# Kernel optimization log

Measured on AMD Instinct MI355X. Metric: run time of the kernel, lower is better.

The kernel has to match this reference:

```python
import math
import jax, jax.numpy as jnp
import numpy as np
from jax.scipy.special import gammaln, xlogy

B, N1, N2 = 4, 2048, 512
D, H, DK = 768, 8, 64
DV = D // H        # 96 (dim_value = dim // heads)
NRP = D // H       # 96 num_rel_pos_features (divisible by 6)
DY0 = 1280 + 256   # esm_dim + cell_line_dim
EPS = 1e-5
SCALE = DK ** -0.5


def layer_norm(z, g, b):
    m = jnp.mean(z, -1, keepdims=True)
    v = jnp.mean(jnp.square(z - m), -1, keepdims=True)
    return (z - m) * jax.lax.rsqrt(v + EPS) * g + b


def get_positional_embed(seq_len, feature_size):
    # Enformer-style relative positional features over distances [-(L-1), L-1]
    d = jnp.arange(-seq_len + 1, seq_len)
    ad = jnp.abs(d).astype(jnp.float32)[:, None]  # [2L-1, 1]
    nb = feature_size // 6
    # exponential half-life basis
    max_range = math.log(seq_len) / math.log(2.0)
    half_life = 2.0 ** jnp.linspace(3.0, max_range, nb)
    f_exp = jnp.exp(-math.log(2.0) / half_life * ad)
    # central mask basis
    cw = 2.0 ** jnp.arange(1, nb + 1).astype(jnp.float32) - 1.0
    f_cm = (cw > ad).astype(jnp.float32)
    # gamma pdf basis
    stddev = seq_len / (2.0 * nb)
    start_mean = seq_len / nb
    mean = jnp.linspace(start_mean, float(seq_len), nb)
    conc = (mean / stddev) ** 2
    rate = mean / (stddev ** 2)
    logp = xlogy(conc - 1.0, ad) - rate * ad - (gammaln(conc) - conc * jnp.log(rate))
    prob = jnp.exp(logp) + 1e-8
    f_g = prob / jnp.max(prob, -1, keepdims=True)
    emb = jnp.concatenate([f_exp, f_cm, f_g], -1)  # [2L-1, feature_size/2]
    sign = jnp.sign(d).astype(jnp.float32)[:, None]
    return jnp.concatenate([emb, sign * emb], -1)  # [2L-1, feature_size]


def relative_shift(z):
    # Transformer-XL shift: [b,h,i,2*L-1] -> [b,h,i,L]
    b, h, i, j = z.shape
    z = jnp.pad(z, ((0, 0), (0, 0), (0, 0), (1, 0)))
    z = z.reshape(b, h, j + 1, i)[:, :, 1:, :].reshape(b, h, i, j)
    return z[..., : (j + 2) // 2]


def ffn(z, g, b, w1, b1, w2, b2):
    h = layer_norm(z, g, b)
    h = jax.nn.relu(h @ w1 + b1)
    return z + h @ w2 + b2


def setup_inputs() -> dict:
    key = jax.random.key(0)
    ks = jax.random.split(key, 32)
    p = lambda i, shape, s=0.02: jax.random.normal(ks[i], shape, jnp.float32) * s
    return dict(
        x=jax.random.normal(ks[0], (B, N1, D), jnp.float32),
        y0=jax.random.normal(ks[1], (B, N2, DY0), jnp.float32),
        W_res=p(2, (DY0, D)),
        lnx_g=jnp.ones((D,)), lnx_b=jnp.zeros((D,)),
        lny_g=jnp.ones((D,)), lny_b=jnp.zeros((D,)),
        Wq=p(3, (D, H * DK)), Wk=p(4, (D, H * DK)),
        Wv1=p(5, (D, H * DV)), Wv2=p(6, (D, H * DV)),
        Wo1=p(7, (H * DV, D)), bo1=jnp.zeros((D,)),
        Wo2=p(8, (H * DV, D)), bo2=jnp.zeros((D,)),
        Wrel=p(9, (NRP, H * DK)),
        rel_pos_bias=p(10, (H, DK), 1.0),
        fx_g=jnp.ones((D,)), fx_b=jnp.zeros((D,)),
        fx_w1=p(11, (D, 2 * D)), fx_b1=jnp.zeros((2 * D,)),
        fx_w2=p(12, (2 * D, D)), fx_b2=jnp.zeros((D,)),
        fy_g=jnp.ones((D,)), fy_b=jnp.zeros((D,)),
        fy_w1=p(13, (D, 2 * D)), fy_b1=jnp.zeros((2 * D,)),
        fy_w2=p(14, (2 * D, D)), fy_b2=jnp.zeros((D,)),
    )


def reference(x, y0, W_res, lnx_g, lnx_b, lny_g, lny_b, Wq, Wk, Wv1, Wv2,
              Wo1, bo1, Wo2, bo2, Wrel, rel_pos_bias,
              fx_g, fx_b, fx_w1, fx_b1, fx_w2, fx_b2,
              fy_g, fy_b, fy_w1, fy_b1, fy_w2, fy_b2):
    b, n1, _ = x.shape
    n2 = y0.shape[1]
    y = y0 @ W_res                               # res_proj (first layer)
    x1 = layer_norm(x, lnx_g, lnx_b)
    y1 = layer_norm(y, lny_g, lny_b)

    q = (x1 @ Wq).reshape(b, n1, H, DK).transpose(0, 2, 1, 3) * SCALE
    k = (y1 @ Wk).reshape(b, n2, H, DK).transpose(0, 2, 1, 3)
    v2 = (y1 @ Wv2).reshape(b, n2, H, DV).transpose(0, 2, 1, 3)

    content = jnp.einsum('bhid,bhjd->bhij', q, k)  # [b,h,n1,n2]

    pos = get_positional_embed(n1, NRP)            # [2*n1-1, NRP]
    rel_q = (pos @ Wrel).reshape(2 * n1 - 1, H, DK).transpose(1, 0, 2)
    kb = k * SCALE + rel_pos_bias[None, :, None, :]
    rel = jnp.einsum('bhjd,hmd->bhjm', kb, rel_q)  # [b,h,n2,2*n1-1]
    rel = relative_shift(rel)                      # [b,h,n2,n1]
    logits = content + rel.transpose(0, 1, 3, 2)

    attn = jax.nn.softmax(logits, -1)
    out1 = jnp.einsum('bhij,bhjd->bhid', attn, v2)
    out1 = out1.transpose(0, 2, 1, 3).reshape(b, n1, H * DV)
    x2 = out1 @ Wo1 + bo1

    v1 = (x1 @ Wv1).reshape(b, n1, H, DV).transpose(0, 2, 1, 3)
    out2 = jnp.einsum('bhij,bhid->bhjd', attn, v1)  # attn^T @ v1
    out2 = out2.transpose(0, 2, 1, 3).reshape(b, n2, H * DV)
    y2 = out2 @ Wo2 + bo2

    x4 = x + x2
    x5 = ffn(x4, fx_g, fx_b, fx_w1, fx_b1, fx_w2, fx_b2)
    y4 = y2 + y
    y5 = ffn(y4, fy_g, fy_b, fy_w1, fy_b1, fy_w2, fy_b2)
    return (x5, y5)
```

## Files before the change

kernel.cpp:

```cpp
#include <hip/hip_runtime.h>
#include <hip/hip_bf16.h>
#include <math.h>

typedef __hip_bfloat16 bf16;
typedef short s16x8 __attribute__((ext_vector_type(8)));
typedef short s16x4 __attribute__((ext_vector_type(4)));
typedef float f32x4 __attribute__((ext_vector_type(4)));

#define B_    4
#define N1_   2048
#define N2_   512
#define D_    768
#define H_    8
#define DK_   64
#define DV_   96
#define NPOS_ 4095
#define SCALE_ 0.125f

__device__ __forceinline__ float b2f(bf16 v) { return __bfloat162float(v); }
__device__ __forceinline__ bf16  f2b(float v) { return __float2bfloat16(v); }
__device__ __forceinline__ float us2f(unsigned short u) {
    return __uint_as_float(((unsigned int)u) << 16);
}
__device__ __forceinline__ unsigned short f2bu(float v) {
    bf16 t = __float2bfloat16(v);
    return *reinterpret_cast<unsigned short*>(&t);
}
__device__ __forceinline__ float ldf(const float* p) { return *p; }
__device__ __forceinline__ float ldf(const bf16* p)  { return __bfloat162float(*p); }
__device__ __forceinline__ void stf(float* p, float v) { *p = v; }
__device__ __forceinline__ void stf(bf16* p, float v)  { *p = f2b(v); }
#define MFMA16(a, b, c) __builtin_amdgcn_mfma_f32_16x16x32_bf16((a), (b), (c), 0, 0, 0)

__device__ __forceinline__ void gl16(const unsigned short* g, unsigned short* l) {
    __builtin_amdgcn_global_load_lds(
        (const __attribute__((address_space(1))) unsigned int*)g,
        (__attribute__((address_space(3))) unsigned int*)l, 16, 0, 0);
}

struct PackT {
    const float* src[12];
    unsigned K[12], N[12], dbase[12], drow[12];
    unsigned t0[13];
};

__global__ __launch_bounds__(256) void packT_kernel(PackT pa, bf16* __restrict__ dst)
{
    int bid = blockIdx.x, s = 0;
    while (s < 11 && bid >= (int)pa.t0[s + 1]) s++;
    int t = bid - (int)pa.t0[s];
    unsigned K = pa.K[s], N = pa.N[s];
    unsigned ntk = K >> 5;
    unsigned k0 = (t % ntk) << 5, n0 = (t / ntk) << 6;
    __shared__ float tile[32][65];
    const float* src = pa.src[s];
    int tid = threadIdx.x;
    {
        int e = tid * 8, k = e >> 6, n = e & 63;
        const float* p = src + (size_t)(k0 + k) * N + n0 + n;
#pragma unroll
        for (int j = 0; j < 8; j++) tile[k][n + j] = p[j];
    }
    __syncthreads();
    {
        int f = tid * 8, n = f >> 5, k = f & 31;
        bf16* q = dst + (size_t)pa.dbase[s] + (size_t)(n0 + n) * pa.drow[s] + k0 + k;
#pragma unroll
        for (int j = 0; j < 8; j++) q[j] = f2b(tile[k + j][n]);
    }
}

__global__ __launch_bounds__(256) void cvt8_kernel(
    const float* __restrict__ in, bf16* __restrict__ out)
{
    int i = (blockIdx.x * 256 + threadIdx.x) * 8;
    f32x4 a = *reinterpret_cast<const f32x4*>(in + i);
    f32x4 b = *reinterpret_cast<const f32x4*>(in + i + 4);
    s16x8 w;
#pragma unroll
    for (int j = 0; j < 4; j++) {
        w[j] = (short)f2bu(a[j]);
        w[4 + j] = (short)f2bu(b[j]);
    }
    *reinterpret_cast<s16x8*>((unsigned short*)out + i) = w;
}

template <typename T>
__global__ __launch_bounds__(64) void lnfull_kernel(
    const T* __restrict__ in, const float* __restrict__ g,
    const float* __restrict__ b, bf16* __restrict__ out)
{
    int row = blockIdx.x, lane = threadIdx.x;
    const T* p = in + (size_t)row * D_;
    float v[12];
    float s = 0.f;
#pragma unroll
    for (int i = 0; i < 12; i++) { v[i] = ldf(p + lane + i * 64); s += v[i]; }
#pragma unroll
    for (int o = 32; o > 0; o >>= 1) s += __shfl_down(s, o);
    float mean = __shfl(s, 0) * (1.f / 768.f);
    float var = 0.f;
#pragma unroll
    for (int i = 0; i < 12; i++) { float d = v[i] - mean; var += d * d; }
#pragma unroll
    for (int o = 32; o > 0; o >>= 1) var += __shfl_down(var, o);
    float rstd = rsqrtf(__shfl(var, 0) * (1.f / 768.f) + 1e-5f);
    bf16* q = out + (size_t)row * D_;
#pragma unroll
    for (int i = 0; i < 12; i++) {
        int c = lane + i * 64;
        q[c] = f2b((v[i] - mean) * rstd * g[c] + b[c]);
    }
}

__global__ __launch_bounds__(256, 4) void wres_splitk_kernel(
    const bf16* __restrict__ Av, const bf16* __restrict__ BwT,
    float* __restrict__ Cp)
{
    __shared__ __align__(16) unsigned short As[128 * 64];
    __shared__ __align__(16) unsigned short Bs[128 * 64];
    const int K = 1536;
    int tid = threadIdx.x, wave = tid >> 6, lane = tid & 63;
    int lc = lane & 15, kq = lane >> 4;
    int wm = (wave & 1) * 64, wn = (wave >> 1) * 64;
    int bid = blockIdx.x;
    int sbid = (bid & 7) * 48 + (bid >> 3);
    int s = sbid / 96, t = sbid % 96;
    int bm = (t / 6) * 128, bn = (t % 6) * 128;
    int ks = s * 384;
    f32x4 acc[4][4] = {};
    int grow = tid >> 3, gcol = (tid & 7) * 8;
    const unsigned short* ag = (const unsigned short*)Av + (size_t)(bm + grow) * K + gcol;
    const unsigned short* bg = (const unsigned short*)BwT + (size_t)(bn + grow) * K + gcol;
    unsigned short* asl = As + wave * 512;
    unsigned short* bsl = Bs + wave * 512;

    for (int k0 = ks; k0 < ks + 384; k0 += 64) {
#pragma unroll
        for (int it = 0; it < 4; it++) {
            gl16(ag + (size_t)(it * 32) * K + k0, asl + it * 2048);
            gl16(bg + (size_t)(it * 32) * K + k0, bsl + it * 2048);
        }
        __syncthreads();
#pragma unroll
        for (int kh = 0; kh < 2; kh++) {
            s16x8 af[4], bf[4];
#pragma unroll
            for (int mt = 0; mt < 4; mt++)
                af[mt] = *reinterpret_cast<const s16x8*>(&As[(wm + mt * 16 + lc) * 64 + kh * 32 + kq * 8]);
#pragma unroll
            for (int nt = 0; nt < 4; nt++)
                bf[nt] = *reinterpret_cast<const s16x8*>(&Bs[(wn + nt * 16 + lc) * 64 + kh * 32 + kq * 8]);
#pragma unroll
            for (int mt = 0; mt < 4; mt++)
#pragma unroll
                for (int nt = 0; nt < 4; nt++)
                    acc[mt][nt] = MFMA16(af[mt], bf[nt], acc[mt][nt]);
        }
        __syncthreads();
    }

    float* out = Cp + (size_t)s * (2048 * 768);
#pragma unroll
    for (int mt = 0; mt < 4; mt++)
#pragma unroll
        for (int nt = 0; nt < 4; nt++) {
            int n = bn + wn + nt * 16 + lc;
#pragma unroll
            for (int r = 0; r < 4; r++) {
                int m = bm + wm + mt * 16 + kq * 4 + r;
                out[(size_t)m * 768 + n] = acc[mt][nt][r];
            }
        }
}

__global__ __launch_bounds__(64) void lnred4_kernel(
    const float* __restrict__ Cp, const float* __restrict__ g,
    const float* __restrict__ b, float* __restrict__ yb, bf16* __restrict__ y1)
{
    int row = blockIdx.x, lane = threadIdx.x;
    const size_t SL = (size_t)2048 * 768;
    const float* p = Cp + (size_t)row * 768;
    float* yo = yb + (size_t)row * 768;
    float v[12];
    float s = 0.f;
#pragma unroll
    for (int i = 0; i < 12; i++) {
        int c = lane + i * 64;
        float t = p[c] + p[SL + c] + p[2 * SL + c] + p[3 * SL + c];
        v[i] = t; s += t;
        yo[c] = t;
    }
#pragma unroll
    for (int o = 32; o > 0; o >>= 1) s += __shfl_down(s, o);
    float mean = __shfl(s, 0) * (1.f / 768.f);
    float var = 0.f;
#pragma unroll
    for (int i = 0; i < 12; i++) { float d = v[i] - mean; var += d * d; }
#pragma unroll
    for (int o = 32; o > 0; o >>= 1) var += __shfl_down(var, o);
    float rstd = rsqrtf(__shfl(var, 0) * (1.f / 768.f) + 1e-5f);
    bf16* q = y1 + (size_t)row * D_;
#pragma unroll
    for (int i = 0; i < 12; i++) {
        int c = lane + i * 64;
        q[c] = f2b((v[i] - mean) * rstd * g[c] + b[c]);
    }
}

template <int AM, typename TC, typename TR>
__device__ __forceinline__ void gemm128_body(
    unsigned short* As, unsigned short* Bs, int tid,
    const void* Av, const bf16* BwT, TC* C, int M, int N, int K,
    const float* bias, int relu, const TR* res,
    bf16* Cq, bf16* Cv, bf16* Cq2, const float* qbias2,
    float sscale, int vshift, int bm, int bn)
{
    int wave = tid >> 6, lane = tid & 63;
    int lc = lane & 15, kq = lane >> 4;
    int wm = (wave & 1) * 64, wn = (wave >> 1) * 64;
    f32x4 acc[4][4] = {};
    int grow = tid >> 3, gcol = (tid & 7) * 8;
    const unsigned short* bg = (const unsigned short*)BwT + (size_t)(bn + grow) * K + gcol;
    unsigned short* asl = As + wave * 512;
    unsigned short* bsl = Bs + wave * 512;
    const size_t SL = (size_t)B_ * N2_ * 768;

    for (int k0 = 0; k0 < K; k0 += 64) {
        if (AM == 0) {
            const unsigned short* ag = (const unsigned short*)Av + (size_t)(bm + grow) * K + k0 + gcol;
#pragma unroll
            for (int it = 0; it < 4; it++)
                gl16(ag + (size_t)(it * 32) * K, asl + it * 2048);
        } else {
#pragma unroll
            for (int it = 0; it < 4; it++) {
                const unsigned short* a0 = (const unsigned short*)Av
                    + (size_t)(bm + grow + it * 32) * K + k0 + gcol;
                s16x8 v0 = *reinterpret_cast<const s16x8*>(a0);
                s16x8 v1 = *reinterpret_cast<const s16x8*>(a0 + SL);
                s16x8 v2 = *reinterpret_cast<const s16x8*>(a0 + 2 * SL);
                s16x8 v3 = *reinterpret_cast<const s16x8*>(a0 + 3 * SL);
                s16x8 w;
#pragma unroll
                for (int j = 0; j < 8; j++)
                    w[j] = (short)f2bu(us2f((unsigned short)v0[j]) + us2f((unsigned short)v1[j]) +
                                       us2f((unsigned short)v2[j]) + us2f((unsigned short)v3[j]));
                *reinterpret_cast<s16x8*>(&As[(grow + it * 32) * 64 + gcol]) = w;
            }
        }
#pragma unroll
        for (int it = 0; it < 4; it++)
            gl16(bg + (size_t)(it * 32) * K + k0, bsl + it * 2048);
        __syncthreads();
#pragma unroll
        for (int kh = 0; kh < 2; kh++) {
            s16x8 af[4], bf[4];
#pragma unroll
            for (int mt = 0; mt < 4; mt++)
                af[mt] = *reinterpret_cast<const s16x8*>(&As[(wm + mt * 16 + lc) * 64 + kh * 32 + kq * 8]);
#pragma unroll
            for (int nt = 0; nt < 4; nt++)
                bf[nt] = *reinterpret_cast<const s16x8*>(&Bs[(wn + nt * 16 + lc) * 64 + kh * 32 + kq * 8]);
#pragma unroll
            for (int mt = 0; mt < 4; mt++)
#pragma unroll
                for (int nt = 0; nt < 4; nt++)
                    acc[mt][nt] = MFMA16(af[mt], bf[nt], acc[mt][nt]);
        }
        __syncthreads();
    }

#pragma unroll
    for (int mt = 0; mt < 4; mt++) {
#pragma unroll
        for (int nt = 0; nt < 4; nt++) {
            int n = bn + wn + nt * 16 + lc;
            float bv = (!Cq && bias) ? bias[n] : 0.f;
#pragma unroll
            for (int r = 0; r < 4; r++) {
                int m = bm + wm + mt * 16 + kq * 4 + r;
                float vr = acc[mt][nt][r];
                if (Cq) {
                    int rows = 1 << vshift;
                    int bb = m >> vshift, rr = m & (rows - 1);
                    if (n < 512) {
                        size_t off = (((size_t)bb * 8 + (n >> 6)) * rows + rr) * 64 + (n & 63);
                        Cq[off] = f2b(vr * sscale);
                        if (Cq2) Cq2[off] = f2b(vr * SCALE_ + qbias2[n]);
                    } else {
                        int nn = n - 512, hh = nn / 96, dv = nn - hh * 96;
                        Cv[(((size_t)bb * 8 + hh) * rows + rr) * 96 + dv] = f2b(vr);
                    }
                } else {
                    float v = vr + bv;
                    if (relu) v = fmaxf(v, 0.f);
                    size_t off = (size_t)m * N + n;
                    if (res) v += ldf(res + off);
                    stf(C + off, v);
                }
            }
        }
    }
}

struct GP {
    const void* Av; const bf16* BwT; void* C;
    int M, N, K;
    const float* bias; int relu; const void* res;
    bf16 *Cq, *Cv, *Cq2; const float* qbias2;
    float sscale; int vshift; int nbx, nwg;
};

template <int AMA, int AMB, typename TC, typename TR>
__global__ __launch_bounds__(256, 4) void dual128_kernel(GP a, GP b)
{
    __shared__ __align__(16) unsigned short As[128 * 64];
    __shared__ __align__(16) unsigned short Bs[128 * 64];
    int tid = threadIdx.x;
    int bid = blockIdx.x;
    if (bid < a.nwg) {
        int sbid = (a.nwg & 7) ? bid : ((bid & 7) * (a.nwg >> 3) + (bid >> 3));
        gemm128_body<AMA, TC, TR>(As, Bs, tid, a.Av, a.BwT, (TC*)a.C,
            a.M, a.N, a.K, a.bias, a.relu, (const TR*)a.res,
            a.Cq, a.Cv, a.Cq2, a.qbias2, a.sscale, a.vshift,
            (sbid / a.nbx) * 128, (sbid % a.nbx) * 128);
    } else {
        int lb = bid - a.nwg;
        int sbid = (b.nwg & 7) ? lb : ((lb & 7) * (b.nwg >> 3) + (lb >> 3));
        gemm128_body<AMB, TC, TR>(As, Bs, tid, b.Av, b.BwT, (TC*)b.C,
            b.M, b.N, b.K, b.bias, b.relu, (const TR*)b.res,
            b.Cq, b.Cv, b.Cq2, b.qbias2, b.sscale, b.vshift,
            (sbid / b.nbx) * 128, (sbid % b.nbx) * 128);
    }
}

__global__ __launch_bounds__(256, 4) void dual3_kernel(GP a, GP b,
    const bf16* __restrict__ relA, const bf16* __restrict__ relB,
    bf16* __restrict__ relC)
{
    __shared__ __align__(16) unsigned short As[128 * 64];
    __shared__ __align__(16) unsigned short Bs[128 * 64];
    int tid = threadIdx.x;
    int bid = blockIdx.x;
    if (bid < a.nwg) {
        int sbid = (bid & 7) * (a.nwg >> 3) + (bid >> 3);
        gemm128_body<0, bf16, float>(As, Bs, tid, a.Av, a.BwT, (bf16*)a.C,
            a.M, a.N, a.K, a.bias, a.relu, (const float*)a.res,
            a.Cq, a.Cv, a.Cq2, a.qbias2, a.sscale, a.vshift,
            (sbid / a.nbx) * 128, (sbid % a.nbx) * 128);
    } else if (bid < a.nwg + b.nwg) {
        int lb = bid - a.nwg;
        int sbid = (lb & 7) * (b.nwg >> 3) + (lb >> 3);
        gemm128_body<0, bf16, float>(As, Bs, tid, b.Av, b.BwT, (bf16*)b.C,
            b.M, b.N, b.K, b.bias, b.relu, (const float*)b.res,
            b.Cq, b.Cv, b.Cq2, b.qbias2, b.sscale, b.vshift,
            (sbid / b.nbx) * 128, (sbid % b.nbx) * 128);
    } else {
        int lb = bid - a.nwg - b.nwg;
        int slb = (lb & 7) * 64 + (lb >> 3);
        int bm = (slb >> 3) * 64, bn = (slb & 7) * 64;
        const int M = NPOS_, N = 512, K = 96;
        unsigned short (*A6)[40] = (unsigned short (*)[40])As;
        unsigned short (*B6)[40] = (unsigned short (*)[40])Bs;
        int wave = tid >> 6, lane = tid & 63;
        f32x4 acc[4] = {};
        int am = tid >> 2, ak = (tid & 3) * 8;
        int bn_ = tid & 63, bk = (tid >> 6) * 8;
        for (int k0 = 0; k0 < K; k0 += 32) {
            s16x8 va = {};
            if (bm + am < M)
                va = *reinterpret_cast<const s16x8*>(
                    (const unsigned short*)relA + (size_t)(bm + am) * K + k0 + ak);
            *reinterpret_cast<s16x8*>(&A6[am][ak]) = va;
            *reinterpret_cast<s16x8*>(&B6[bn_][bk]) =
                *reinterpret_cast<const s16x8*>(
                    (const unsigned short*)relB + (size_t)(bn + bn_) * K + k0 + bk);
            __syncthreads();
            s16x8 af = *reinterpret_cast<const s16x8*>(&A6[wave * 16 + (lane & 15)][(lane >> 4) * 8]);
#pragma unroll
            for (int ns = 0; ns < 4; ns++) {
                s16x8 bf = *reinterpret_cast<const s16x8*>(&B6[ns * 16 + (lane & 15)][(lane >> 4) * 8]);
                acc[ns] = MFMA16(af, bf, acc[ns]);
            }
            __syncthreads();
        }
        int col = lane & 15, rg = (lane >> 4) * 4;
#pragma unroll
        for (int ns = 0; ns < 4; ns++) {
            int n = bn + ns * 16 + col;
#pragma unroll
            for (int r = 0; r < 4; r++) {
                int m = bm + wave * 16 + rg + r;
                if (m < M) relC[(size_t)m * N + n] = f2b(acc[ns][r]);
            }
        }
    }
}

__global__ __launch_bounds__(64) void pos_kernel(bf16* __restrict__ pos)
{
    int m = blockIdx.x * 64 + threadIdx.x;
    if (m >= NPOS_) return;
    float dist = (float)(m - 2047);
    float ad = fabsf(dist);
    float sgn = (dist > 0.f) ? 1.f : ((dist < 0.f) ? -1.f : 0.f);
    float f[48];
#pragma unroll
    for (int t = 0; t < 16; t++) {
        float hl = exp2f(3.f + (8.f / 15.f) * (float)t);
        f[t] = expf(-0.69314718056f / hl * ad);
    }
#pragma unroll
    for (int t = 0; t < 16; t++) {
        float cw = exp2f((float)(t + 1)) - 1.f;
        f[16 + t] = (cw > ad) ? 1.f : 0.f;
    }
    float pr[16];
    float mx = 0.f;
    if (ad < 0.5f) {
#pragma unroll
        for (int t = 0; t < 16; t++) pr[t] = 1e-8f;
        mx = 1e-8f;
    } else {
        float lad = logf(ad);
#pragma unroll
        for (int t = 0; t < 16; t++) {
            float mean = 128.f * (float)(t + 1);
            float cc = (mean / 64.f) * (mean / 64.f);
            float rate = mean * (1.f / 4096.f);
            float logp = (cc - 1.f) * lad - rate * ad - (lgammaf(cc) - cc * logf(rate));
            float p = expf(logp) + 1e-8f;
            pr[t] = p;
            mx = fmaxf(mx, p);
        }
    }
#pragma unroll
    for (int t = 0; t < 16; t++) f[32 + t] = pr[t] / mx;

    bf16* o = pos + (size_t)m * 96;
#pragma unroll
    for (int c = 0; c < 48; c++) { o[c] = f2b(f[c]); o[48 + c] = f2b(sgn * f[c]); }
}

#define TP_ 344
__global__ __launch_bounds__(256) void tshift_kernel(
    const bf16* __restrict__ kbb, const bf16* __restrict__ relq,
    bf16* __restrict__ tsh, int base, int plen)
{
    int mc = blockIdx.x, jt = blockIdx.y, bh = blockIdx.z;
    int mbase = mc << 8, jg0 = jt << 6, h = bh & 7;
    int iwin0 = mbase + jg0 - 511 - base;
    if (iwin0 + 318 < 0 || iwin0 >= plen) return;
    int a0 = iwin0 & 7;
    int iwa = iwin0 - a0;
    __shared__ unsigned short Tl[64][TP_];
    int tid = threadIdx.x, wave = tid >> 6, lane = tid & 63;
    int lc = lane & 15, kq = lane >> 4;

    const bf16* ap = kbb + ((size_t)bh * N2_ + jg0 + wave * 16 + lc) * 64 + kq * 8;
    s16x8 af0 = *reinterpret_cast<const s16x8*>(ap);
    s16x8 af1 = *reinterpret_cast<const s16x8*>(ap + 32);

    int jrow = wave * 16 + kq * 4;
#pragma unroll
    for (int sub = 0; sub < 2; sub++) {
        int m0 = mbase + sub * 128;
        f32x4 tacc[8] = {};
#pragma unroll
        for (int ns = 0; ns < 8; ns++) {
            const bf16* rp = relq + (size_t)(m0 + ns * 16 + lc) * 512 + h * 64 + kq * 8;
            s16x8 rf0 = *reinterpret_cast<const s16x8*>(rp);
            s16x8 rf1 = *reinterpret_cast<const s16x8*>(rp + 32);
            tacc[ns] = MFMA16(af0, rf0, tacc[ns]);
            tacc[ns] = MFMA16(af1, rf1, tacc[ns]);
        }
#pragma unroll
        for (int ns = 0; ns < 8; ns++)
#pragma unroll
            for (int r = 0; r < 4; r++) {
                int col = sub * 128 + ns * 16 + lc + jrow + r + a0;
                Tl[jrow + r][col] = f2bu(tacc[ns][r]);
            }
    }
    __syncthreads();

    int row = tid >> 2, q = tid & 3;
    int cstart = row + a0;
    bf16* out = tsh + ((size_t)bh * N2_ + jg0 + row) * (size_t)plen;
#pragma unroll
    for (int s = 0; s < 11; s++) {
        int c = (q + s * 4) * 8;
        int i = iwa + c;
        if (c >= cstart && c + 8 <= cstart + 256 && i >= 0 && i + 8 <= plen) {
            *reinterpret_cast<s16x8*>(out + i) =
                *reinterpret_cast<const s16x8*>(&Tl[row][c]);
        } else {
#pragma unroll
            for (int e = 0; e < 8; e++) {
                int ce = c + e, ie = i + e;
                if (ce >= cstart && ce < cstart + 256 && ie >= 0 && ie < plen)
                    out[ie] = *reinterpret_cast<const bf16*>(&Tl[row][ce]);
            }
        }
    }
}

__global__ __launch_bounds__(256) void attn1_kernel(
    const bf16* __restrict__ qb, const bf16* __restrict__ kb,
    const bf16* __restrict__ tsh, const bf16* __restrict__ v2,
    bf16* __restrict__ out1, float* __restrict__ mst, float* __restrict__ lst,
    int base, int tpitch)
{
    int bh = blockIdx.y;
    int b = bh >> 3, h = bh & 7;
    int i0 = base + blockIdx.x * 64;
    __shared__ __align__(16) unsigned short Ts[64][72];
    __shared__ __align__(16) unsigned short Ps[64][72];
    __shared__ __align__(16) unsigned short Vs[96][72];
    int tid = threadIdx.x, wave = tid >> 6, lane = tid & 63;
    int lc = lane & 15, kq = lane >> 4;
    int ibase = wave * 16 + kq * 4;

    const bf16* qp = qb + ((size_t)bh * N1_ + i0 + wave * 16 + lc) * 64 + kq * 8;
    s16x8 qf0 = *reinterpret_cast<const s16x8*>(qp);
    s16x8 qf1 = *reinterpret_cast<const s16x8*>(qp + 32);

    int trow = tid >> 2, tchunk = tid & 3;
    const unsigned short* tb0 = (const unsigned short*)tsh
        + ((size_t)bh * N2_ + trow) * tpitch + (i0 - base) + tchunk * 16;
    const unsigned short* vb0 = (const unsigned short*)v2
        + ((size_t)bh * N2_ + trow) * 96 + tchunk * 24;

    float m_run[4], l_run[4];
#pragma unroll
    for (int r = 0; r < 4; r++) { m_run[r] = -1e30f; l_run[r] = 0.f; }
    f32x4 oacc[6] = {};

    for (int j0 = 0; j0 < N2_; j0 += 64) {
        __syncthreads();
        {
            const unsigned short* p = tb0 + (size_t)j0 * tpitch;
            *reinterpret_cast<s16x8*>(&Ts[trow][tchunk * 16]) =
                *reinterpret_cast<const s16x8*>(p);
            *reinterpret_cast<s16x8*>(&Ts[trow][tchunk * 16 + 8]) =
                *reinterpret_cast<const s16x8*>(p + 8);
        }
        {
            const unsigned short* p = vb0 + (size_t)j0 * 96;
            s16x8 w0 = *reinterpret_cast<const s16x8*>(p);
            s16x8 w1 = *reinterpret_cast<const s16x8*>(p + 8);
            s16x8 w2 = *reinterpret_cast<const s16x8*>(p + 16);
            int vd = tchunk * 24;
#pragma unroll
            for (int s = 0; s < 8; s++) Vs[vd + s][trow] = (unsigned short)w0[s];
#pragma unroll
            for (int s = 0; s < 8; s++) Vs[vd + 8 + s][trow] = (unsigned short)w1[s];
#pragma unroll
            for (int s = 0; s < 8; s++) Vs[vd + 16 + s][trow] = (unsigned short)w2[s];
        }
        __syncthreads();

        f32x4 cacc[4] = {};
#pragma unroll
        for (int ns = 0; ns < 4; ns++) {
            const bf16* kp = kb + ((size_t)bh * N2_ + j0 + ns * 16 + lc) * 64 + kq * 8;
            s16x8 kf0 = *reinterpret_cast<const s16x8*>(kp);
            s16x8 kf1 = *reinterpret_cast<const s16x8*>(kp + 32);
            cacc[ns] = MFMA16(qf0, kf0, cacc[ns]);
            cacc[ns] = MFMA16(qf1, kf1, cacc[ns]);
        }
        float Lv[4][4];
#pragma unroll
        for (int ns = 0; ns < 4; ns++) {
            int jloc = ns * 16 + lc;
            s16x4 tv = *reinterpret_cast<const s16x4*>(&Ts[jloc][ibase]);
#pragma unroll
            for (int r = 0; r < 4; r++)
                Lv[ns][r] = cacc[ns][r] + us2f((unsigned short)tv[r]);
        }
#pragma unroll
        for (int r = 0; r < 4; r++) {
            float v = fmaxf(fmaxf(Lv[0][r], Lv[1][r]), fmaxf(Lv[2][r], Lv[3][r]));
            v = fmaxf(v, __shfl_xor(v, 1));
            v = fmaxf(v, __shfl_xor(v, 2));
            v = fmaxf(v, __shfl_xor(v, 4));
            v = fmaxf(v, __shfl_xor(v, 8));
            float mn = fmaxf(m_run[r], v);
            float alpha = __expf(m_run[r] - mn);
            m_run[r] = mn;
            float s = 0.f;
#pragma unroll
            for (int ns = 0; ns < 4; ns++) {
                float p = __expf(Lv[ns][r] - mn);
                Lv[ns][r] = p;
                s += p;
            }
            s += __shfl_xor(s, 1);
            s += __shfl_xor(s, 2);
            s += __shfl_xor(s, 4);
            s += __shfl_xor(s, 8);
            l_run[r] = l_run[r] * alpha + s;
#pragma unroll
            for (int ns6 = 0; ns6 < 6; ns6++) oacc[ns6][r] *= alpha;
        }
#pragma unroll
        for (int ns = 0; ns < 4; ns++)
#pragma unroll
            for (int r = 0; r < 4; r++)
                Ps[ibase + r][ns * 16 + lc] = f2bu(Lv[ns][r]);
#pragma unroll
        for (int kk = 0; kk < 2; kk++) {
            s16x8 pf = *reinterpret_cast<const s16x8*>(&Ps[wave * 16 + lc][kq * 8 + kk * 32]);
#pragma unroll
            for (int ns6 = 0; ns6 < 6; ns6++) {
                s16x8 vf = *reinterpret_cast<const s16x8*>(&Vs[ns6 * 16 + lc][kq * 8 + kk * 32]);
                oacc[ns6] = MFMA16(pf, vf, oacc[ns6]);
            }
        }
    }

    float invl[4];
#pragma unroll
    for (int r = 0; r < 4; r++) invl[r] = 1.f / l_run[r];
#pragma unroll
    for (int ns6 = 0; ns6 < 6; ns6++)
#pragma unroll
        for (int r = 0; r < 4; r++)
            out1[(size_t)(b * N1_ + i0 + ibase + r) * 768 + h * 96 + ns6 * 16 + lc]
                = f2b(oacc[ns6][r] * invl[r]);
    if (lc == 0) {
#pragma unroll
        for (int r = 0; r < 4; r++) {
            mst[(size_t)bh * N1_ + i0 + ibase + r] = m_run[r];
            lst[(size_t)bh * N1_ + i0 + ibase + r] = l_run[r];
        }
    }
}

__global__ __launch_bounds__(256) void attn2_kernel(
    const bf16* __restrict__ qb, const bf16* __restrict__ kb,
    const bf16* __restrict__ tsh, const bf16* __restrict__ v1,
    bf16* __restrict__ out2b, const float* __restrict__ mst,
    const float* __restrict__ lst, int base, int tpitch)
{
    int jt = blockIdx.x, bh = blockIdx.y;
    int b = bh >> 3, h = bh & 7;
    int ib = base + blockIdx.z * 512;
    bf16* out2 = out2b + (size_t)(ib >> 9) * ((size_t)B_ * N2_ * 768);
    int j0 = jt * 64;
    __shared__ __align__(16) unsigned short Ts[64][72];
    __shared__ __align__(16) unsigned short Ps[64][72];
    __shared__ __align__(16) unsigned short Vs[96][72];
    int tid = threadIdx.x, wave = tid >> 6, lane = tid & 63;
    int lc = lane & 15, kq = lane >> 4;
    int ibase = wave * 16 + kq * 4;

    s16x8 kf0[4], kf1[4];
#pragma unroll
    for (int ns = 0; ns < 4; ns++) {
        const bf16* kp = kb + ((size_t)bh * N2_ + j0 + ns * 16 + lc) * 64 + kq * 8;
        kf0[ns] = *reinterpret_cast<const s16x8*>(kp);
        kf1[ns] = *reinterpret_cast<const s16x8*>(kp + 32);
    }

    int trow = tid >> 2, tchunk = tid & 3;
    const unsigned short* tb0 = (const unsigned short*)tsh
        + ((size_t)bh * N2_ + j0 + trow) * tpitch + tchunk * 16;
    const unsigned short* vb0 = (const unsigned short*)v1
        + ((size_t)bh * N1_ + trow) * 96 + tchunk * 24;

    f32x4 oacc[6] = {};
    for (int i0 = ib; i0 < ib + 512; i0 += 64) {
        __syncthreads();
        {
            const unsigned short* p = tb0 + (i0 - base);
            *reinterpret_cast<s16x8*>(&Ts[trow][tchunk * 16]) =
                *reinterpret_cast<const s16x8*>(p);
            *reinterpret_cast<s16x8*>(&Ts[trow][tchunk * 16 + 8]) =
                *reinterpret_cast<const s16x8*>(p + 8);
        }
        {
            const unsigned short* p = vb0 + (size_t)i0 * 96;
            s16x8 w0 = *reinterpret_cast<const s16x8*>(p);
            s16x8 w1 = *reinterpret_cast<const s16x8*>(p + 8);
            s16x8 w2 = *reinterpret_cast<const s16x8*>(p + 16);
            int vd = tchunk * 24;
#pragma unroll
            for (int s = 0; s < 8; s++) Vs[vd + s][trow] = (unsigned short)w0[s];
#pragma unroll
            for (int s = 0; s < 8; s++) Vs[vd + 8 + s][trow] = (unsigned short)w1[s];
#pragma unroll
            for (int s = 0; s < 8; s++) Vs[vd + 16 + s][trow] = (unsigned short)w2[s];
        }
        __syncthreads();

        const bf16* qp = qb + ((size_t)bh * N1_ + i0 + wave * 16 + lc) * 64 + kq * 8;
        s16x8 qf0 = *reinterpret_cast<const s16x8*>(qp);
        s16x8 qf1 = *reinterpret_cast<const s16x8*>(qp + 32);
        f32x4 cacc[4] = {};
#pragma unroll
        for (int ns = 0; ns < 4; ns++) {
            cacc[ns] = MFMA16(qf0, kf0[ns], cacc[ns]);
            cacc[ns] = MFMA16(qf1, kf1[ns], cacc[ns]);
        }
        float mi[4], invli[4];
#pragma unroll
        for (int r = 0; r < 4; r++) {
            mi[r] = mst[(size_t)bh * N1_ + i0 + ibase + r];
            invli[r] = 1.f / lst[(size_t)bh * N1_ + i0 + ibase + r];
        }
#pragma unroll
        for (int ns = 0; ns < 4; ns++) {
            int jloc = ns * 16 + lc;
            s16x4 tv = *reinterpret_cast<const s16x4*>(&Ts[jloc][ibase]);
            s16x4 pw;
#pragma unroll
            for (int r = 0; r < 4; r++) {
                float L = cacc[ns][r] + us2f((unsigned short)tv[r]);
                pw[r] = (short)f2bu(__expf(L - mi[r]) * invli[r]);
            }
            *reinterpret_cast<s16x4*>(&Ps[jloc][ibase]) = pw;
        }
        __syncthreads();
#pragma unroll
        for (int kk = 0; kk < 2; kk++) {
            s16x8 pf = *reinterpret_cast<const s16x8*>(&Ps[wave * 16 + lc][kq * 8 + kk * 32]);
#pragma unroll
            for (int ns6 = 0; ns6 < 6; ns6++) {
                s16x8 vf = *reinterpret_cast<const s16x8*>(&Vs[ns6 * 16 + lc][kq * 8 + kk * 32]);
                oacc[ns6] = MFMA16(pf, vf, oacc[ns6]);
            }
        }
    }

#pragma unroll
    for (int ns6 = 0; ns6 < 6; ns6++)
#pragma unroll
        for (int r = 0; r < 4; r++)
            out2[(size_t)(b * N2_ + j0 + ibase + r) * 768 + h * 96 + ns6 * 16 + lc]
                = f2b(oacc[ns6][r]);
}

extern "C" void kernel_launch(void* const* d_in, const int* in_sizes, int n_in,
                              void* d_out, int out_size, void* d_ws, size_t ws_size,
                              hipStream_t stream)
{
    (void)in_sizes; (void)n_in; (void)out_size;
    const float* x      = (const float*)d_in[0];
    const float* y0     = (const float*)d_in[1];
    const float* Wres   = (const float*)d_in[2];
    const float* lnx_g  = (const float*)d_in[3];
    const float* lnx_b  = (const float*)d_in[4];
    const float* lny_g  = (const float*)d_in[5];
    const float* lny_b  = (const float*)d_in[6];
    const float* Wq     = (const float*)d_in[7];
    const float* Wk     = (const float*)d_in[8];
    const float* Wv1    = (const float*)d_in[9];
    const float* Wv2    = (const float*)d_in[10];
    const float* Wo1    = (const float*)d_in[11];
    const float* bo1    = (const float*)d_in[12];
    const float* Wo2    = (const float*)d_in[13];
    const float* bo2    = (const float*)d_in[14];
    const float* Wrel   = (const float*)d_in[15];
    const float* rel_pb = (const float*)d_in[16];
    const float* fx_g   = (const float*)d_in[17];
    const float* fx_b   = (const float*)d_in[18];
    const float* fx_w1  = (const float*)d_in[19];
    const float* fx_b1  = (const float*)d_in[20];
    const float* fx_w2  = (const float*)d_in[21];
    const float* fx_b2  = (const float*)d_in[22];
    const float* fy_g   = (const float*)d_in[23];
    const float* fy_b   = (const float*)d_in[24];
    const float* fy_w1  = (const float*)d_in[25];
    const float* fy_b1  = (const float*)d_in[26];
    const float* fy_w2  = (const float*)d_in[27];
    const float* fy_b2  = (const float*)d_in[28];

    float* out_x = (float*)d_out;
    float* out_y = out_x + (size_t)B_ * N1_ * D_;
    bf16* out1 = (bf16*)d_out;

    char* W = (char*)d_ws;
    size_t o = 0;
    auto alloc = [&](size_t bytes) { char* p = W + o; o += (bytes + 255) & ~(size_t)255; return p; };
    bf16*   qb   = (bf16*)alloc((size_t)B_ * N1_ * 512 * 2);
    bf16*   kb   = (bf16*)alloc((size_t)B_ * N2_ * 512 * 2);
    bf16*   posb = (bf16*)alloc((size_t)NPOS_ * 96 * 2);
    bf16*   relq = (bf16*)alloc((size_t)NPOS_ * 512 * 2);
    bf16*   v1b  = (bf16*)alloc((size_t)B_ * N1_ * 768 * 2);
    bf16*   hx2  = (bf16*)alloc((size_t)B_ * N1_ * 768 * 2);
    bf16*   v2b  = (bf16*)alloc((size_t)B_ * N2_ * 768 * 2);
    float*  yb   = (float*)alloc((size_t)B_ * N2_ * 768 * 4);
    bf16*   kbbb = (bf16*)alloc((size_t)B_ * N2_ * 512 * 2);
    bf16*   wpool= (bf16*)alloc((size_t)9093120 * 2);
    float*  mst  = (float*)alloc((size_t)B_ * H_ * N1_ * 4);
    float*  lst  = (float*)alloc((size_t)B_ * H_ * N1_ * 4);

    size_t x1y1 = ((size_t)B_ * N1_ * 768 + (size_t)B_ * N2_ * 768) * 2;
    size_t rem = ws_size > o ? ws_size - o : 0;
    int plen = 512;
    if (rem >= (size_t)32 * 512 * 2048 * 2 + 1024) plen = 2048;
    else if (rem >= (size_t)32 * 512 * 1024 * 2 + 1024) plen = 1024;
    size_t tshB = (size_t)32 * 512 * (size_t)plen * 2;
    bf16* tshb = (bf16*)alloc(tshB > x1y1 ? tshB : x1y1);
    bf16* x1 = tshb;
    bf16* y1 = x1 + (size_t)B_ * N1_ * 768;

    bf16* y0b = qb;
    float* Cp = (float*)v1b;
    bf16* x4 = qb;
    bf16* y4 = v2b;
    bf16* hx = v1b;
    bf16* out2h = hx2;
    bf16* hy = (bf16*)yb;
    bf16* x4ln = x1;
    bf16* y4ln = y1;

    const unsigned OW_RES = 0, OW_QV1 = 1179648, OW_KV2 = 2162688, OW_O1 = 3145728,
                   OW_O2 = 3735552, OW_REL = 4325376, OW_FXW1 = 4374528,
                   OW_FXW2 = 5554176, OW_FYW1 = 6733824, OW_FYW2 = 7913472;

    PackT pa;
    const float* srcs[12] = {Wres, Wq, Wv1, Wk, Wv2, Wo1, Wo2, Wrel,
                             fx_w1, fx_w2, fy_w1, fy_w2};
    unsigned Ks[12] = {1536, 768, 768, 768, 768, 768, 768, 96, 768, 1536, 768, 1536};
    unsigned Nss[12] = {768, 512, 768, 512, 768, 768, 768, 512, 1536, 768, 1536, 768};
    unsigned dbs[12] = {OW_RES, OW_QV1, OW_QV1 + 393216, OW_KV2, OW_KV2 + 393216,
                        OW_O1, OW_O2, OW_REL, OW_FXW1, OW_FXW2, OW_FYW1, OW_FYW2};
    unsigned drs[12] = {1536, 768, 768, 768, 768, 768, 768, 96, 768, 1536, 768, 1536};
    unsigned cum = 0;
    for (int i = 0; i < 12; i++) {
        pa.src[i] = srcs[i]; pa.K[i] = Ks[i]; pa.N[i] = Nss[i];
        pa.dbase[i] = dbs[i]; pa.drow[i] = drs[i];
        pa.t0[i] = cum;
        cum += (Ks[i] >> 5) * (Nss[i] >> 6);
    }
    pa.t0[12] = cum;

    dim3 blk(256);
    packT_kernel<<<cum, blk, 0, stream>>>(pa, wpool);
    cvt8_kernel<<<(B_ * N2_ * 1536) / 2048, blk, 0, stream>>>(y0, y0b);
    pos_kernel<<<(NPOS_ + 63) / 64, 64, 0, stream>>>(posb);
    lnfull_kernel<float><<<B_ * N1_, 64, 0, stream>>>(x, lnx_g, lnx_b, x1);
    wres_splitk_kernel<<<384, blk, 0, stream>>>(y0b, wpool + OW_RES, Cp);
    lnred4_kernel<<<B_ * N2_, 64, 0, stream>>>(Cp, lny_g, lny_b, yb, y1);
    {
        GP a{x1, wpool + OW_QV1, nullptr, B_ * N1_, 1280, D_,
             nullptr, 0, nullptr, qb, v1b, nullptr, nullptr, SCALE_, 11, 10, 640};
        GP b{y1, wpool + OW_KV2, nullptr, B_ * N2_, 1280, D_,
             nullptr, 0, nullptr, kb, v2b, kbbb, rel_pb, 1.f, 9, 10, 160};
        dual3_kernel<<<1312, blk, 0, stream>>>(a, b, posb, wpool + OW_REL, relq);
    }
    for (int base = 0; base < N1_; base += plen) {
        tshift_kernel<<<dim3(10, 8, 32), blk, 0, stream>>>(kbbb, relq, tshb, base, plen);
        attn1_kernel<<<dim3(plen / 64, 32), blk, 0, stream>>>(
            qb, kb, tshb, v2b, out1, mst, lst, base, plen);
        attn2_kernel<<<dim3(8, 32, plen / 512), blk, 0, stream>>>(
            qb, kb, tshb, v1b, out2h, mst, lst, base, plen);
    }
    {
        GP a{out1, wpool + OW_O1, x4, B_ * N1_, D_, D_,
             bo1, 0, x, nullptr, nullptr, nullptr, nullptr, 0.f, 0, 6, 384};
        GP b{out2h, wpool + OW_O2, y4, B_ * N2_, D_, D_,
             bo2, 0, yb, nullptr, nullptr, nullptr, nullptr, 0.f, 0, 6, 96};
        dual128_kernel<0, 2, bf16, float><<<480, blk, 0, stream>>>(a, b);
    }
    lnfull_kernel<bf16><<<B_ * N1_, 64, 0, stream>>>(x4, fx_g, fx_b, x4ln);
    lnfull_kernel<bf16><<<B_ * N2_, 64, 0, stream>>>(y4, fy_g, fy_b, y4ln);
    {
        GP a{x4ln, wpool + OW_FXW1, hx, B_ * N1_, 1536, D_,
             fx_b1, 1, nullptr, nullptr, nullptr, nullptr, nullptr, 0.f, 0, 12, 768};
        GP b{y4ln, wpool + OW_FYW1, hy, B_ * N2_, 1536, D_,
             fy_b1, 1, nullptr, nullptr, nullptr, nullptr, nullptr, 0.f, 0, 12, 192};
        dual128_kernel<0, 0, bf16, float><<<960, blk, 0, stream>>>(a, b);
    }
    {
        GP a{hx, wpool + OW_FXW2, out_x, B_ * N1_, D_, 1536,
             fx_b2, 0, x4, nullptr, nullptr, nullptr, nullptr, 0.f, 0, 6, 384};
        GP b{hy, wpool + OW_FYW2, out_y, B_ * N2_, D_, 1536,
             fy_b2, 0, y4, nullptr, nullptr, nullptr, nullptr, 0.f, 0, 6, 96};
        dual128_kernel<0, 0, float, bf16><<<480, blk, 0, stream>>>(a, b);
    }
}
```

Baseline: 556.4 us.

## Merge independent prologue and epilogue kernels into combined block-partitioned launches

Merges weight packing, y0 conversion and positional embedding into one launch, and folds the x layernorm into the residual split-K GEMM launch as extra blocks. On the last chunk, the Wo1 output projection runs as extra blocks of the attn2 kernel, and the x4 layernorm runs alongside the Wo2 projection. The aim is to remove launch overhead and idle tail time by overlapping independent work within single grids. The risk is that o2lnx4 reads x4 while it is written by the Wo1 blocks of the previous launch, which is fine across stream order, but mixing block types can lower occupancy, since the merged kernels use 32KB of shared memory and launch bounds of 4.

```diff
diff --git a/kernel.cpp b/kernel.cpp
--- a/kernel.cpp
+++ b/kernel.cpp
@@ -38,92 +38,152 @@
         (__attribute__((address_space(3))) unsigned int*)l, 16, 0, 0);
 }
 
+template <typename T>
+__device__ __forceinline__ void ln_wave(
+    const T* __restrict__ in, const float* __restrict__ g,
+    const float* __restrict__ b, bf16* __restrict__ out, int row, int lane)
+{
+    const T* p = in + (size_t)row * D_;
+    float v[12];
+    float s = 0.f;
+#pragma unroll
+    for (int i = 0; i < 12; i++) { v[i] = ldf(p + lane + i * 64); s += v[i]; }
+#pragma unroll
+    for (int o = 32; o > 0; o >>= 1) s += __shfl_down(s, o);
+    float mean = __shfl(s, 0) * (1.f / 768.f);
+    float var = 0.f;
+#pragma unroll
+    for (int i = 0; i < 12; i++) { float d = v[i] - mean; var += d * d; }
+#pragma unroll
+    for (int o = 32; o > 0; o >>= 1) var += __shfl_down(var, o);
+    float rstd = rsqrtf(__shfl(var, 0) * (1.f / 768.f) + 1e-5f);
+    bf16* q = out + (size_t)row * D_;
+#pragma unroll
+    for (int i = 0; i < 12; i++) {
+        int c = lane + i * 64;
+        q[c] = f2b((v[i] - mean) * rstd * g[c] + b[c]);
+    }
+}
+
+template <typename T>
+__global__ __launch_bounds__(64) void lnfull_kernel(
+    const T* __restrict__ in, const float* __restrict__ g,
+    const float* __restrict__ b, bf16* __restrict__ out)
+{
+    ln_wave<T>(in, g, b, out, blockIdx.x, threadIdx.x);
+}
+
+__device__ __forceinline__ void pos_row(int m, bf16* __restrict__ pos)
+{
+    float dist = (float)(m - 2047);
+    float ad = fabsf(dist);
+    float sgn = (dist > 0.f) ? 1.f : ((dist < 0.f) ? -1.f : 0.f);
+    float f[48];
+#pragma unroll
+    for (int t = 0; t < 16; t++) {
+        float hl = exp2f(3.f + (8.f / 15.f) * (float)t);
+        f[t] = expf(-0.69314718056f / hl * ad);
+    }
+#pragma unroll
+    for (int t = 0; t < 16; t++) {
+        float cw = exp2f((float)(t + 1)) - 1.f;
+        f[16 + t] = (cw > ad) ? 1.f : 0.f;
+    }
+    float pr[16];
+    float mx = 0.f;
+    if (ad < 0.5f) {
+#pragma unroll
+        for (int t = 0; t < 16; t++) pr[t] = 1e-8f;
+        mx = 1e-8f;
+    } else {
+        float lad = logf(ad);
+#pragma unroll
+        for (int t = 0; t < 16; t++) {
+            float mean = 128.f * (float)(t + 1);
+            float cc = (mean / 64.f) * (mean / 64.f);
+            float rate = mean * (1.f / 4096.f);
+            float logp = (cc - 1.f) * lad - rate * ad - (lgammaf(cc) - cc * logf(rate));
+            float p = expf(logp) + 1e-8f;
+            pr[t] = p;
+            mx = fmaxf(mx, p);
+        }
+    }
+#pragma unroll
+    for (int t = 0; t < 16; t++) f[32 + t] = pr[t] / mx;
+    bf16* o = pos + (size_t)m * 96;
+#pragma unroll
+    for (int c = 0; c < 48; c++) { o[c] = f2b(f[c]); o[48 + c] = f2b(sgn * f[c]); }
+}
+
 struct PackT {
     const float* src[12];
     unsigned K[12], N[12], dbase[12], drow[12];
     unsigned t0[13];
 };
 
-__global__ __launch_bounds__(256) void packT_kernel(PackT pa, bf16* __restrict__ dst)
-{
-    int bid = blockIdx.x, s = 0;
-    while (s < 11 && bid >= (int)pa.t0[s + 1]) s++;
-    int t = bid - (int)pa.t0[s];
-    unsigned K = pa.K[s], N = pa.N[s];
-    unsigned ntk = K >> 5;
-    unsigned k0 = (t % ntk) << 5, n0 = (t / ntk) << 6;
+__global__ __launch_bounds__(256) void mega0_kernel(
+    PackT pa, bf16* __restrict__ dst,
+    const float* __restrict__ y0, bf16* __restrict__ y0b,
+    bf16* __restrict__ posb, int nP, int nC)
+{
     __shared__ float tile[32][65];
-    const float* src = pa.src[s];
-    int tid = threadIdx.x;
-    {
-        int e = tid * 8, k = e >> 6, n = e & 63;
-        const float* p = src + (size_t)(k0 + k) * N + n0 + n;
-#pragma unroll
-        for (int j = 0; j < 8; j++) tile[k][n + j] = p[j];
-    }
-    __syncthreads();
-    {
-        int f = tid * 8, n = f >> 5, k = f & 31;
-        bf16* q = dst + (size_t)pa.dbase[s] + (size_t)(n0 + n) * pa.drow[s] + k0 + k;
-#pragma unroll
-        for (int j = 0; j < 8; j++) q[j] = f2b(tile[k + j][n]);
-    }
-}
-
-__global__ __launch_bounds__(256) void cvt8_kernel(
-    const float* __restrict__ in, bf16* __restrict__ out)
-{
-    int i = (blockIdx.x * 256 + threadIdx.x) * 8;
-    f32x4 a = *reinterpret_cast<const f32x4*>(in + i);
-    f32x4 b = *reinterpret_cast<const f32x4*>(in + i + 4);
-    s16x8 w;
-#pragma unroll
-    for (int j = 0; j < 4; j++) {
-        w[j] = (short)f2bu(a[j]);
-        w[4 + j] = (short)f2bu(b[j]);
-    }
-    *reinterpret_cast<s16x8*>((unsigned short*)out + i) = w;
-}
-
-template <typename T>
-__global__ __launch_bounds__(64) void lnfull_kernel(
-    const T* __restrict__ in, const float* __restrict__ g,
-    const float* __restrict__ b, bf16* __restrict__ out)
-{
-    int row = blockIdx.x, lane = threadIdx.x;
-    const T* p = in + (size_t)row * D_;
-    float v[12];
-    float s = 0.f;
-#pragma unroll
-    for (int i = 0; i < 12; i++) { v[i] = ldf(p + lane + i * 64); s += v[i]; }
-#pragma unroll
-    for (int o = 32; o > 0; o >>= 1) s += __shfl_down(s, o);
-    float mean = __shfl(s, 0) * (1.f / 768.f);
-    float var = 0.f;
-#pragma unroll
-    for (int i = 0; i < 12; i++) { float d = v[i] - mean; var += d * d; }
-#pragma unroll
-    for (int o = 32; o > 0; o >>= 1) var += __shfl_down(var, o);
-    float rstd = rsqrtf(__shfl(var, 0) * (1.f / 768.f) + 1e-5f);
-    bf16* q = out + (size_t)row * D_;
-#pragma unroll
-    for (int i = 0; i < 12; i++) {
-        int c = lane + i * 64;
-        q[c] = f2b((v[i] - mean) * rstd * g[c] + b[c]);
-    }
-}
-
-__global__ __launch_bounds__(256, 4) void wres_splitk_kernel(
+    int bid = blockIdx.x, tid = threadIdx.x;
+    if (bid < nP) {
+        int s = 0;
+        while (s < 11 && bid >= (int)pa.t0[s + 1]) s++;
+        int t = bid - (int)pa.t0[s];
+        unsigned K = pa.K[s], N = pa.N[s];
+        unsigned ntk = K >> 5;
+        unsigned k0 = (t % ntk) << 5, n0 = (t / ntk) << 6;
+        const float* src = pa.src[s];
+        {
+            int e = tid * 8, k = e >> 6, n = e & 63;
+            const float* p = src + (size_t)(k0 + k) * N + n0 + n;
+#pragma unroll
+            for (int j = 0; j < 8; j++) tile[k][n + j] = p[j];
+        }
+        __syncthreads();
+        {
+            int f = tid * 8, n = f >> 5, k = f & 31;
+            bf16* q = dst + (size_t)pa.dbase[s] + (size_t)(n0 + n) * pa.drow[s] + k0 + k;
+#pragma unroll
+            for (int j = 0; j < 8; j++) q[j] = f2b(tile[k + j][n]);
+        }
+    } else if (bid < nP + nC) {
+        int i = ((bid - nP) * 256 + tid) * 8;
+        f32x4 a = *reinterpret_cast<const f32x4*>(y0 + i);
+        f32x4 c = *reinterpret_cast<const f32x4*>(y0 + i + 4);
+        s16x8 w;
+#pragma unroll
+        for (int j = 0; j < 4; j++) {
+            w[j] = (short)f2bu(a[j]);
+            w[4 + j] = (short)f2bu(c[j]);
+        }
+        *reinterpret_cast<s16x8*>((unsigned short*)y0b + i) = w;
+    } else {
+        int m = (bid - nP - nC) * 256 + tid;
+        if (m < NPOS_) pos_row(m, posb);
+    }
+}
+
+__global__ __launch_bounds__(256, 4) void wresln_kernel(
     const bf16* __restrict__ Av, const bf16* __restrict__ BwT,
-    float* __restrict__ Cp)
-{
-    __shared__ __align__(16) unsigned short As[128 * 64];
-    __shared__ __align__(16) unsigned short Bs[128 * 64];
+    float* __restrict__ Cp, const float* __restrict__ x,
+    const float* __restrict__ lng, const float* __restrict__ lnb,
+    bf16* __restrict__ x1)
+{
+    __shared__ __align__(16) unsigned short U[16384];
+    int bid = blockIdx.x, tid = threadIdx.x;
+    if (bid >= 384) {
+        ln_wave<float>(x, lng, lnb, x1, (bid - 384) * 4 + (tid >> 6), tid & 63);
+        return;
+    }
+    unsigned short* As = U;
+    unsigned short* Bs = U + 8192;
     const int K = 1536;
-    int tid = threadIdx.x, wave = tid >> 6, lane = tid & 63;
+    int wave = tid >> 6, lane = tid & 63;
     int lc = lane & 15, kq = lane >> 4;
     int wm = (wave & 1) * 64, wn = (wave >> 1) * 64;
-    int bid = blockIdx.x;
     int sbid = (bid & 7) * 48 + (bid >> 3);
     int s = sbid / 96, t = sbid % 96;
     int bm = (t / 6) * 128, bn = (t % 6) * 128;
@@ -398,51 +458,6 @@
     }
 }
 
-__global__ __launch_bounds__(64) void pos_kernel(bf16* __restrict__ pos)
-{
-    int m = blockIdx.x * 64 + threadIdx.x;
-    if (m >= NPOS_) return;
-    float dist = (float)(m - 2047);
-    float ad = fabsf(dist);
-    float sgn = (dist > 0.f) ? 1.f : ((dist < 0.f) ? -1.f : 0.f);
-    float f[48];
-#pragma unroll
-    for (int t = 0; t < 16; t++) {
-        float hl = exp2f(3.f + (8.f / 15.f) * (float)t);
-        f[t] = expf(-0.69314718056f / hl * ad);
-    }
-#pragma unroll
-    for (int t = 0; t < 16; t++) {
-        float cw = exp2f((float)(t + 1)) - 1.f;
-        f[16 + t] = (cw > ad) ? 1.f : 0.f;
-    }
-    float pr[16];
-    float mx = 0.f;
-    if (ad < 0.5f) {
-#pragma unroll
-        for (int t = 0; t < 16; t++) pr[t] = 1e-8f;
-        mx = 1e-8f;
-    } else {
-        float lad = logf(ad);
-#pragma unroll
-        for (int t = 0; t < 16; t++) {
-            float mean = 128.f * (float)(t + 1);
-            float cc = (mean / 64.f) * (mean / 64.f);
-            float rate = mean * (1.f / 4096.f);
-            float logp = (cc - 1.f) * lad - rate * ad - (lgammaf(cc) - cc * logf(rate));
-            float p = expf(logp) + 1e-8f;
-            pr[t] = p;
-            mx = fmaxf(mx, p);
-        }
-    }
-#pragma unroll
-    for (int t = 0; t < 16; t++) f[32 + t] = pr[t] / mx;
-
-    bf16* o = pos + (size_t)m * 96;
-#pragma unroll
-    for (int c = 0; c < 48; c++) { o[c] = f2b(f[c]); o[48 + c] = f2b(sgn * f[c]); }
-}
-
 #define TP_ 344
 __global__ __launch_bounds__(256) void tshift_kernel(
     const bf16* __restrict__ kbb, const bf16* __restrict__ relq,
@@ -638,21 +653,22 @@
     }
 }
 
-__global__ __launch_bounds__(256) void attn2_kernel(
+__device__ __forceinline__ void attn2_body(
+    unsigned short* U, int tid, int jt, int bh, int zq,
     const bf16* __restrict__ qb, const bf16* __restrict__ kb,
     const bf16* __restrict__ tsh, const bf16* __restrict__ v1,
     bf16* __restrict__ out2b, const float* __restrict__ mst,
     const float* __restrict__ lst, int base, int tpitch)
 {
-    int jt = blockIdx.x, bh = blockIdx.y;
+    typedef unsigned short (*arr72)[72];
+    arr72 Ts = (arr72)U;
+    arr72 Ps = (arr72)(U + 4608);
+    arr72 Vs = (arr72)(U + 9216);
     int b = bh >> 3, h = bh & 7;
-    int ib = base + blockIdx.z * 512;
+    int ib = base + zq * 512;
     bf16* out2 = out2b + (size_t)(ib >> 9) * ((size_t)B_ * N2_ * 768);
     int j0 = jt * 64;
-    __shared__ __align__(16) unsigned short Ts[64][72];
-    __shared__ __align__(16) unsigned short Ps[64][72];
-    __shared__ __align__(16) unsigned short Vs[96][72];
-    int tid = threadIdx.x, wave = tid >> 6, lane = tid & 63;
+    int wave = tid >> 6, lane = tid & 63;
     int lc = lane & 15, kq = lane >> 4;
     int ibase = wave * 16 + kq * 4;
 
@@ -740,6 +756,45 @@
         for (int r = 0; r < 4; r++)
             out2[(size_t)(b * N2_ + j0 + ibase + r) * 768 + h * 96 + ns6 * 16 + lc]
                 = f2b(oacc[ns6][r]);
+}
+
+__global__ __launch_bounds__(256, 4) void attn2o1_kernel(
+    const bf16* __restrict__ qb, const bf16* __restrict__ kb,
+    const bf16* __restrict__ tsh, const bf16* __restrict__ v1,
+    bf16* __restrict__ out2b, const float* __restrict__ mst,
+    const float* __restrict__ lst, int base, int tpitch, int nA2, GP g1)
+{
+    __shared__ __align__(16) unsigned short U[16384];
+    int bid = blockIdx.x, tid = threadIdx.x;
+    if (bid < nA2) {
+        int jt = bid & 7, bh = (bid >> 3) & 31, zq = bid >> 8;
+        attn2_body(U, tid, jt, bh, zq, qb, kb, tsh, v1, out2b, mst, lst, base, tpitch);
+    } else {
+        int lb = bid - nA2;
+        int sbid = (lb & 7) * (g1.nwg >> 3) + (lb >> 3);
+        gemm128_body<0, bf16, float>(U, U + 8192, tid, g1.Av, g1.BwT, (bf16*)g1.C,
+            g1.M, g1.N, g1.K, g1.bias, g1.relu, (const float*)g1.res,
+            g1.Cq, g1.Cv, g1.Cq2, g1.qbias2, g1.sscale, g1.vshift,
+            (sbid / g1.nbx) * 128, (sbid % g1.nbx) * 128);
+    }
+}
+
+__global__ __launch_bounds__(256, 4) void o2lnx4_kernel(GP g2,
+    const bf16* __restrict__ x4, const float* __restrict__ g,
+    const float* __restrict__ b, bf16* __restrict__ x4ln)
+{
+    __shared__ __align__(16) unsigned short U[16384];
+    int bid = blockIdx.x, tid = threadIdx.x;
+    if (bid < g2.nwg) {
+        int sbid = (bid & 7) * (g2.nwg >> 3) + (bid >> 3);
+        gemm128_body<2, bf16, float>(U, U + 8192, tid, g2.Av, g2.BwT, (bf16*)g2.C,
+            g2.M, g2.N, g2.K, g2.bias, g2.relu, (const float*)g2.res,
+            g2.Cq, g2.Cv, g2.Cq2, g2.qbias2, g2.sscale, g2.vshift,
+            (sbid / g2.nbx) * 128, (sbid % g2.nbx) * 128);
+    } else {
+        int row = (bid - g2.nwg) * 4 + (tid >> 6);
+        ln_wave<bf16>(x4, g, b, x4ln, row, tid & 63);
+    }
 }
 
 extern "C" void kernel_launch(void* const* d_in, const int* in_sizes, int n_in,
@@ -839,11 +894,9 @@
     pa.t0[12] = cum;
 
     dim3 blk(256);
-    packT_kernel<<<cum, blk, 0, stream>>>(pa, wpool);
-    cvt8_kernel<<<(B_ * N2_ * 1536) / 2048, blk, 0, stream>>>(y0, y0b);
-    pos_kernel<<<(NPOS_ + 63) / 64, 64, 0, stream>>>(posb);
-    lnfull_kernel<float><<<B_ * N1_, 64, 0, stream>>>(x, lnx_g, lnx_b, x1);
-    wres_splitk_kernel<<<384, blk, 0, stream>>>(y0b, wpool + OW_RES, Cp);
+    const int nC = (B_ * N2_ * 1536) / 2048;
+    mega0_kernel<<<cum + nC + 16, blk, 0, stream>>>(pa, wpool, y0, y0b, posb, cum, nC);
+    wresln_kernel<<<2432, blk, 0, stream>>>(y0b, wpool + OW_RES, Cp, x, lnx_g, lnx_b, x1);
     lnred4_kernel<<<B_ * N2_, 64, 0, stream>>>(Cp, lny_g, lny_b, yb, y1);
     {
         GP a{x1, wpool + OW_QV1, nullptr, B_ * N1_, 1280, D_,
@@ -852,21 +905,22 @@
              nullptr, 0, nullptr, kb, v2b, kbbb, rel_pb, 1.f, 9, 10, 160};
         dual3_kernel<<<1312, blk, 0, stream>>>(a, b, posb, wpool + OW_REL, relq);
     }
+    GP g1{out1, wpool + OW_O1, x4, B_ * N1_, D_, D_,
+          bo1, 0, x, nullptr, nullptr, nullptr, nullptr, 0.f, 0, 6, 384};
     for (int base = 0; base < N1_; base += plen) {
         tshift_kernel<<<dim3(10, 8, 32), blk, 0, stream>>>(kbbb, relq, tshb, base, plen);
         attn1_kernel<<<dim3(plen / 64, 32), blk, 0, stream>>>(
             qb, kb, tshb, v2b, out1, mst, lst, base, plen);
-        attn2_kernel<<<dim3(8, 32, plen / 512), blk, 0, stream>>>(
-            qb, kb, tshb, v1b, out2h, mst, lst, base, plen);
+        int nA2 = 256 * (plen / 512);
+        int last = (base + plen >= N1_) ? g1.nwg : 0;
+        attn2o1_kernel<<<nA2 + last, blk, 0, stream>>>(
+            qb, kb, tshb, v1b, out2h, mst, lst, base, plen, nA2, g1);
     }
     {
-        GP a{out1, wpool + OW_O1, x4, B_ * N1_, D_, D_,
-             bo1, 0, x, nullptr, nullptr, nullptr, nullptr, 0.f, 0, 6, 384};
-        GP b{out2h, wpool + OW_O2, y4, B_ * N2_, D_, D_,
-             bo2, 0, yb, nullptr, nullptr, nullptr, nullptr, 0.f, 0, 6, 96};
-        dual128_kernel<0, 2, bf16, float><<<480, blk, 0, stream>>>(a, b);
-    }
-    lnfull_kernel<bf16><<<B_ * N1_, 64, 0, stream>>>(x4, fx_g, fx_b, x4ln);
+        GP g2{out2h, wpool + OW_O2, y4, B_ * N2_, D_, D_,
+              bo2, 0, yb, nullptr, nullptr, nullptr, nullptr, 0.f, 0, 6, 96};
+        o2lnx4_kernel<<<96 + 2048, blk, 0, stream>>>(g2, x4, fx_g, fx_b, x4ln);
+    }
     lnfull_kernel<bf16><<<B_ * N2_, 64, 0, stream>>>(y4, fy_g, fy_b, y4ln);
     {
         GP a{x4ln, wpool + OW_FXW1, hx, B_ * N1_, 1536, D_,
```

New measurement: 579.6 us. 4.2% more time.
